# Kernel optimization log

Hardware: AMD Instinct MI355X
Metric: run time of the kernel (lower is better)

## Reference

```python
import jax, jax.numpy as jnp
import numpy as np

COMMITMENT_COST = 0.25

def setup_inputs() -> dict:
    key = jax.random.key(0)
    k1, k2 = jax.random.split(key)
    B, K, D = 32768, 4096, 256
    inputs = jax.random.normal(k1, (B, D), dtype=jnp.float32)
    embedding = jax.random.normal(k2, (K, D), dtype=jnp.float32) * (1.0 / np.sqrt(D))
    return {"inputs": inputs, "embedding": embedding}

def reference(inputs, embedding):
    distances = (
        jnp.sum(inputs * inputs, axis=1, keepdims=True)
        + jnp.sum(embedding * embedding, axis=1)
        - 2.0 * jnp.einsum("bd,kd->bk", inputs, embedding)
    )
    encoding_indices = jnp.argmin(distances, axis=1)  # [B]
    # one-hot @ embedding == gather
    quantized = embedding[encoding_indices]  # [B, D]
    # Eval-mode loss (module in inference mode): q_latent + commitment * e_latent
    e_latent_loss = jnp.mean((inputs - jax.lax.stop_gradient(quantized)) ** 2)
    q_latent_loss = jnp.mean((quantized - jax.lax.stop_gradient(inputs)) ** 2)
    loss = q_latent_loss + COMMITMENT_COST * e_latent_loss
    # Straight-through estimator
    quantized_st = inputs + jax.lax.stop_gradient(quantized - inputs)
    return (quantized_st, loss, encoding_indices)
```

## Files before the change

kernel.cpp:

```cpp
#include <hip/hip_runtime.h>

constexpr int Bsz = 32768;
constexpr int Ksz = 4096;
constexpr int Dsz = 256;

constexpr int KD = 512;
constexpr int NSLABS = 4;
constexpr int CTILES = 8;
constexpr int NCAND = 8;
constexpr int NFBLK = Bsz / 4;
constexpr float TAU = 1e-3f;

typedef __attribute__((ext_vector_type(8))) short short8;
typedef __attribute__((ext_vector_type(4))) float f32x4;

__device__ __forceinline__ unsigned short f2bf(float f) {
  unsigned u = __float_as_uint(f);
  u += 0x7fffu + ((u >> 16) & 1u);
  return (unsigned short)(u >> 16);
}
__device__ __forceinline__ float bf2f(unsigned short h) {
  return __uint_as_float(((unsigned)h) << 16);
}

__global__ __launch_bounds__(256) void vq_prep_x(const float* __restrict__ X,
                                                 unsigned short* __restrict__ X2) {
  const int tid = blockIdx.x * 256 + threadIdx.x;
  const int row = tid >> 6;
  const int d4 = tid & 63;
  const float4 v = *reinterpret_cast<const float4*>(X + (size_t)row * Dsz + d4 * 4);
  ushort4 h, l;
  h.x = f2bf(v.x); l.x = f2bf(v.x - bf2f(h.x));
  h.y = f2bf(v.y); l.y = f2bf(v.y - bf2f(h.y));
  h.z = f2bf(v.z); l.z = f2bf(v.z - bf2f(h.z));
  h.w = f2bf(v.w); l.w = f2bf(v.w - bf2f(h.w));
  *reinterpret_cast<ushort4*>(X2 + (size_t)row * KD + d4 * 4) = h;
  *reinterpret_cast<ushort4*>(X2 + (size_t)row * KD + 256 + d4 * 4) = l;
}

__global__ __launch_bounds__(256) void vq_prep_e(const float* __restrict__ E,
                                                 unsigned short* __restrict__ E2,
                                                 float* __restrict__ enorm) {
  const int wid = threadIdx.x >> 6;
  const int lane = threadIdx.x & 63;
  const int k = blockIdx.x * 4 + wid;
  const float4 v = *reinterpret_cast<const float4*>(E + (size_t)k * Dsz + lane * 4);
  ushort4 h, l;
  h.x = f2bf(v.x); l.x = f2bf(v.x - bf2f(h.x));
  h.y = f2bf(v.y); l.y = f2bf(v.y - bf2f(h.y));
  h.z = f2bf(v.z); l.z = f2bf(v.z - bf2f(h.z));
  h.w = f2bf(v.w); l.w = f2bf(v.w - bf2f(h.w));
  *reinterpret_cast<ushort4*>(E2 + (size_t)k * KD + lane * 4) = h;
  *reinterpret_cast<ushort4*>(E2 + (size_t)k * KD + 256 + lane * 4) = l;
  float s = v.x * v.x + v.y * v.y + v.z * v.z + v.w * v.w;
#pragma unroll
  for (int off = 32; off > 0; off >>= 1) s += __shfl_down(s, off);
  if (lane == 0) enorm[k] = s;
}

__global__ __launch_bounds__(256, 2) void vq_gemm_argmin(
    const unsigned short* __restrict__ X2, const unsigned short* __restrict__ E2,
    const float* __restrict__ enorm, float4* __restrict__ cand) {
  __shared__ unsigned short sA[128 * 64];
  __shared__ unsigned short sB[128 * 64];

  const int t = threadIdx.x;
  const int lane = t & 63;
  const int wid = t >> 6;
  const int wm = wid >> 1, wn = wid & 1;
  const int mb = blockIdx.x & 255;
  const int slab = blockIdx.x >> 8;
  const int row0 = mb * 128;
  const int col0 = slab * 1024;

  const int rr = lane >> 3;
  const int sl = (lane & 7) ^ rr;
  const int sloff = (sl & 3) * 8 + ((sl & 4) << 6);

  const int l15 = lane & 15;
  const int fsel = ((lane >> 4) ^ (lane & 7)) * 8;

  float m1[16], m2[16];
  int i1[16], i2[16];
#pragma unroll
  for (int r = 0; r < 16; ++r) {
    m1[r] = 3.4e38f; m2[r] = 3.4e38f; i1[r] = 0x7fffffff; i2[r] = 0x7fffffff;
  }

  for (int ct = 0; ct < CTILES; ++ct) {
    const int colt = col0 + ct * 128;
    f32x4 acc[4][4];
#pragma unroll
    for (int a = 0; a < 4; ++a)
#pragma unroll
      for (int b = 0; b < 4; ++b) acc[a][b] = f32x4{0.f, 0.f, 0.f, 0.f};

    for (int c = 0; c < 8; ++c) {
      const int kb = c * 32;
      __syncthreads();
      const int rbase = wid * 32;
#pragma unroll
      for (int qi = 0; qi < 4; ++qi) {
        const int r0 = rbase + qi * 8;
        const unsigned short* gA =
            X2 + (size_t)(row0 + r0 + rr) * KD + kb + sloff;
        __builtin_amdgcn_global_load_lds(
            (const __attribute__((address_space(1))) void*)gA,
            (__attribute__((address_space(3))) void*)(sA + r0 * 64), 16, 0, 0);
        const unsigned short* gB =
            E2 + (size_t)(colt + r0 + rr) * KD + kb + sloff;
        __builtin_amdgcn_global_load_lds(
            (const __attribute__((address_space(1))) void*)gB,
            (__attribute__((address_space(3))) void*)(sB + r0 * 64), 16, 0, 0);
      }
      __syncthreads();

      short8 ah[4], bh[4];
#pragma unroll
      for (int a = 0; a < 4; ++a)
        ah[a] = *reinterpret_cast<const short8*>(
            sA + (wm * 64 + a * 16 + l15) * 64 + fsel);
#pragma unroll
      for (int b = 0; b < 4; ++b)
        bh[b] = *reinterpret_cast<const short8*>(
            sB + (wn * 64 + b * 16 + l15) * 64 + fsel);
#pragma unroll
      for (int a = 0; a < 4; ++a)
#pragma unroll
        for (int b = 0; b < 4; ++b)
          acc[a][b] = __builtin_amdgcn_mfma_f32_16x16x32_bf16(ah[a], bh[b], acc[a][b], 0, 0, 0);

      short8 al[4];
#pragma unroll
      for (int a = 0; a < 4; ++a)
        al[a] = *reinterpret_cast<const short8*>(
            sA + (wm * 64 + a * 16 + l15) * 64 + (fsel ^ 32));
#pragma unroll
      for (int a = 0; a < 4; ++a)
#pragma unroll
        for (int b = 0; b < 4; ++b)
          acc[a][b] = __builtin_amdgcn_mfma_f32_16x16x32_bf16(al[a], bh[b], acc[a][b], 0, 0, 0);

      short8 bl[4];
#pragma unroll
      for (int b = 0; b < 4; ++b)
        bl[b] = *reinterpret_cast<const short8*>(
            sB + (wn * 64 + b * 16 + l15) * 64 + (fsel ^ 32));
#pragma unroll
      for (int a = 0; a < 4; ++a)
#pragma unroll
        for (int b = 0; b < 4; ++b)
          acc[a][b] = __builtin_amdgcn_mfma_f32_16x16x32_bf16(ah[a], bl[b], acc[a][b], 0, 0, 0);
    }

#pragma unroll
    for (int b = 0; b < 4; ++b) {
      const int colg = colt + wn * 64 + b * 16 + l15;
      const float en = enorm[colg];
#pragma unroll
      for (int a = 0; a < 4; ++a) {
#pragma unroll
        for (int q = 0; q < 4; ++q) {
          const float s = en - 2.0f * acc[a][b][q];
          const int r = a * 4 + q;
          if (s < m1[r]) {
            m2[r] = m1[r]; i2[r] = i1[r]; m1[r] = s; i1[r] = colg;
          } else if (s < m2[r]) {
            m2[r] = s; i2[r] = colg;
          }
        }
      }
    }
  }

#pragma unroll
  for (int r = 0; r < 16; ++r) {
    float v1 = m1[r], v2 = m2[r];
    int ii1 = i1[r], ii2 = i2[r];
#pragma unroll
    for (int mbit = 1; mbit <= 8; mbit <<= 1) {
      const float ov1 = __shfl_xor(v1, mbit);
      const float ov2 = __shfl_xor(v2, mbit);
      const int oi1 = __shfl_xor(ii1, mbit);
      const int oi2 = __shfl_xor(ii2, mbit);
      if (ov1 < v1 || (ov1 == v1 && oi1 < ii1)) {
        float nv2 = v1; int ni2 = ii1;
        if (ov2 < nv2) { nv2 = ov2; ni2 = oi2; }
        v1 = ov1; ii1 = oi1; v2 = nv2; ii2 = ni2;
      } else if (ov1 < v2) {
        v2 = ov1; ii2 = oi1;
      }
    }
    if (l15 == 0) {
      const int rowg = row0 + wm * 64 + (r >> 2) * 16 + (lane >> 4) * 4 + (r & 3);
      cand[(size_t)rowg * NCAND + slab * 2 + wn] =
          make_float4(v1, __int_as_float(ii1), v2, __int_as_float(ii2));
    }
  }
}

__global__ __launch_bounds__(256) void vq_finalize(
    const float* __restrict__ X, const float* __restrict__ E,
    const float4* __restrict__ cand, float* __restrict__ out,
    float* __restrict__ partial) {
  __shared__ float ls[4];
  const int wid = threadIdx.x >> 6;
  const int lane = threadIdx.x & 63;
  const int b = blockIdx.x * 4 + wid;

  float v1 = 3.4e38f, v2 = 3.4e38f;
  int ii1 = 0x7fffffff, ii2 = 0x7fffffff;
  if (lane < NCAND) {
    const float4 c = cand[(size_t)b * NCAND + lane];
    v1 = c.x; ii1 = __float_as_int(c.y);
    v2 = c.z; ii2 = __float_as_int(c.w);
  }
#pragma unroll
  for (int mbit = 1; mbit <= 4; mbit <<= 1) {
    const float ov1 = __shfl_xor(v1, mbit);
    const float ov2 = __shfl_xor(v2, mbit);
    const int oi1 = __shfl_xor(ii1, mbit);
    const int oi2 = __shfl_xor(ii2, mbit);
    if (ov1 < v1 || (ov1 == v1 && oi1 < ii1)) {
      float nv2 = v1; int ni2 = ii1;
      if (ov2 < nv2) { nv2 = ov2; ni2 = oi2; }
      v1 = ov1; ii1 = oi1; v2 = nv2; ii2 = ni2;
    } else if (ov1 < v2) {
      v2 = ov1; ii2 = oi1;
    }
  }
  v1 = __shfl(v1, 0); v2 = __shfl(v2, 0);
  ii1 = __shfl(ii1, 0); ii2 = __shfl(ii2, 0);

  const float4 x = *reinterpret_cast<const float4*>(X + (size_t)b * Dsz + lane * 4);

  if (v2 - v1 < TAU) {
    const float4 e1 = *reinterpret_cast<const float4*>(E + (size_t)ii1 * Dsz + lane * 4);
    const float4 e2 = *reinterpret_cast<const float4*>(E + (size_t)ii2 * Dsz + lane * 4);
    double d1 = ((double)x.x - e1.x) * ((double)x.x - e1.x) +
                ((double)x.y - e1.y) * ((double)x.y - e1.y) +
                ((double)x.z - e1.z) * ((double)x.z - e1.z) +
                ((double)x.w - e1.w) * ((double)x.w - e1.w);
    double d2 = ((double)x.x - e2.x) * ((double)x.x - e2.x) +
                ((double)x.y - e2.y) * ((double)x.y - e2.y) +
                ((double)x.z - e2.z) * ((double)x.z - e2.z) +
                ((double)x.w - e2.w) * ((double)x.w - e2.w);
#pragma unroll
    for (int mbit = 1; mbit <= 32; mbit <<= 1) {
      d1 += __shfl_xor(d1, mbit);
      d2 += __shfl_xor(d2, mbit);
    }
    if (d2 < d1 || (d2 == d1 && ii2 < ii1)) ii1 = ii2;
  }

  const float4 q = *reinterpret_cast<const float4*>(E + (size_t)ii1 * Dsz + lane * 4);
  *reinterpret_cast<float4*>(out + (size_t)b * Dsz + lane * 4) = q;

  const float dx = x.x - q.x, dy = x.y - q.y, dz = x.z - q.z, dw = x.w - q.w;
  float s2 = dx * dx + dy * dy + dz * dz + dw * dw;
#pragma unroll
  for (int off = 32; off > 0; off >>= 1) s2 += __shfl_down(s2, off);
  if (lane == 0) {
    ls[wid] = s2;
    out[(size_t)Bsz * Dsz + 1 + b] = (float)ii1;
  }
  __syncthreads();
  if (threadIdx.x == 0)
    partial[blockIdx.x] = ls[0] + ls[1] + ls[2] + ls[3];
}

__global__ __launch_bounds__(256) void vq_loss_reduce(const float* __restrict__ partial,
                                                      float* __restrict__ out) {
  __shared__ float ls[4];
  const int wid = threadIdx.x >> 6;
  const int lane = threadIdx.x & 63;
  float s = 0.f;
  for (int i = threadIdx.x; i < NFBLK; i += 256) s += partial[i];
#pragma unroll
  for (int off = 32; off > 0; off >>= 1) s += __shfl_down(s, off);
  if (lane == 0) ls[wid] = s;
  __syncthreads();
  if (threadIdx.x == 0)
    out[(size_t)Bsz * Dsz] = (ls[0] + ls[1] + ls[2] + ls[3]) *
                             (1.25f / ((float)Bsz * (float)Dsz));
}

extern "C" void kernel_launch(void* const* d_in, const int* in_sizes, int n_in,
                              void* d_out, int out_size, void* d_ws, size_t ws_size,
                              hipStream_t stream) {
  const float* X = (const float*)d_in[0];
  const float* E = (const float*)d_in[1];
  float* out = (float*)d_out;

  char* ws = (char*)d_ws;
  float* enorm = (float*)ws;
  unsigned short* X2 = (unsigned short*)(ws + (16 << 10));
  unsigned short* E2 = (unsigned short*)(ws + (16 << 10) + (32 << 20));
  float4* cand = (float4*)(ws + (16 << 10) + (36 << 20));
  float* partial = (float*)(ws + (16 << 10) + (40 << 20));

  vq_prep_x<<<Bsz * 64 / 256, 256, 0, stream>>>(X, X2);
  vq_prep_e<<<Ksz / 4, 256, 0, stream>>>(E, E2, enorm);
  vq_gemm_argmin<<<(Bsz / 128) * NSLABS, 256, 0, stream>>>(X2, E2, enorm, cand);
  vq_finalize<<<NFBLK, 256, 0, stream>>>(X, E, cand, out, partial);
  vq_loss_reduce<<<1, 256, 0, stream>>>(partial, out);
}
```

Before: 384.3 us.

## Restructure argmin GEMM into 256x256 tiles with double-buffered LDS pipeline

The GEMM-argmin kernel moves from 128-row blocks that loop over 1024-column slabs to 512-thread blocks that each compute one 256x256 output tile. LDS staging is double-buffered, with explicit vmcnt waits, barriers and setprio so global-to-LDS loads overlap the MFMAs. The three bf16 split products (hi*hi, lo*hi, hi*lo) are folded into one 12-step K loop through offset macros. Block indices are swizzled for L2 locality, and per-tile top-2 candidates are merged in shared memory, which doubles the candidate count that finalize reduces. The larger tiles raise arithmetic reuse per byte loaded, at the cost of higher register and LDS pressure and a larger candidate buffer.

```diff
diff --git a/kernel.cpp b/kernel.cpp
--- a/kernel.cpp
+++ b/kernel.cpp
@@ -5,9 +5,8 @@
 constexpr int Dsz = 256;
 
 constexpr int KD = 512;
-constexpr int NSLABS = 4;
-constexpr int CTILES = 8;
-constexpr int NCAND = 8;
+constexpr int NT = 12;
+constexpr int NCAND = 16;
 constexpr int NFBLK = Bsz / 4;
 constexpr float TAU = 1e-3f;
 
@@ -58,145 +57,186 @@
   if (lane == 0) enorm[k] = s;
 }
 
-__global__ __launch_bounds__(256, 2) void vq_gemm_argmin(
+__global__ __launch_bounds__(512, 2) void vq_gemm_argmin(
     const unsigned short* __restrict__ X2, const unsigned short* __restrict__ E2,
     const float* __restrict__ enorm, float4* __restrict__ cand) {
-  __shared__ unsigned short sA[128 * 64];
-  __shared__ unsigned short sB[128 * 64];
-
-  const int t = threadIdx.x;
-  const int lane = t & 63;
-  const int wid = t >> 6;
-  const int wm = wid >> 1, wn = wid & 1;
-  const int mb = blockIdx.x & 255;
-  const int slab = blockIdx.x >> 8;
-  const int row0 = mb * 128;
-  const int col0 = slab * 1024;
-
-  const int rr = lane >> 3;
-  const int sl = (lane & 7) ^ rr;
-  const int sloff = (sl & 3) * 8 + ((sl & 4) << 6);
+  __shared__ unsigned short sA[2][256 * 64];
+  __shared__ unsigned short sB[2][256 * 64];
+
+  const int t5 = threadIdx.x;
+  const int lane = t5 & 63;
+  const int wid = t5 >> 6;
+  const int wm = wid >> 2;
+  const int wn = wid & 3;
+
+  const int bid = blockIdx.x;
+  const int swz = (bid & 7) * 256 + (bid >> 3);
+  const int mb = swz >> 4;
+  const int nb = swz & 15;
+  const int row0 = mb * 256;
+  const int col0 = nb * 256;
+
+  const int srow = lane >> 3;
+  const int sslot = (lane & 7) ^ srow;
 
   const int l15 = lane & 15;
-  const int fsel = ((lane >> 4) ^ (lane & 7)) * 8;
-
-  float m1[16], m2[16];
-  int i1[16], i2[16];
-#pragma unroll
-  for (int r = 0; r < 16; ++r) {
-    m1[r] = 3.4e38f; m2[r] = 3.4e38f; i1[r] = 0x7fffffff; i2[r] = 0x7fffffff;
-  }
-
-  for (int ct = 0; ct < CTILES; ++ct) {
-    const int colt = col0 + ct * 128;
-    f32x4 acc[4][4];
-#pragma unroll
-    for (int a = 0; a < 4; ++a)
-#pragma unroll
-      for (int b = 0; b < 4; ++b) acc[a][b] = f32x4{0.f, 0.f, 0.f, 0.f};
-
-    for (int c = 0; c < 8; ++c) {
-      const int kb = c * 32;
-      __syncthreads();
-      const int rbase = wid * 32;
-#pragma unroll
-      for (int qi = 0; qi < 4; ++qi) {
-        const int r0 = rbase + qi * 8;
-        const unsigned short* gA =
-            X2 + (size_t)(row0 + r0 + rr) * KD + kb + sloff;
-        __builtin_amdgcn_global_load_lds(
-            (const __attribute__((address_space(1))) void*)gA,
-            (__attribute__((address_space(3))) void*)(sA + r0 * 64), 16, 0, 0);
-        const unsigned short* gB =
-            E2 + (size_t)(colt + r0 + rr) * KD + kb + sloff;
-        __builtin_amdgcn_global_load_lds(
-            (const __attribute__((address_space(1))) void*)gB,
-            (__attribute__((address_space(3))) void*)(sB + r0 * 64), 16, 0, 0);
+  const int lhi = lane >> 4;
+  const int lx = lane & 7;
+
+  f32x4 acc[8][4];
+#pragma unroll
+  for (int m = 0; m < 8; ++m)
+#pragma unroll
+    for (int n = 0; n < 4; ++n) acc[m][n] = f32x4{0.f, 0.f, 0.f, 0.f};
+
+#define AOF(kt) ((((kt) >> 2) == 1 ? 256 : 0) + ((kt) & 3) * 64)
+#define BOF(kt) ((((kt) >> 2) == 2 ? 256 : 0) + ((kt) & 3) * 64)
+
+#define STAGE(BUFI, AO, BO)                                                    \
+  {                                                                            \
+    _Pragma("unroll") for (int q = 0; q < 4; ++q) {                            \
+      const int r = wid * 32 + q * 8;                                          \
+      __builtin_amdgcn_global_load_lds(                                        \
+          (const __attribute__((address_space(1))) void*)(                     \
+              X2 + (size_t)(row0 + r + srow) * KD + (AO) + sslot * 8),         \
+          (__attribute__((address_space(3))) void*)(&sA[BUFI][r * 64]), 16, 0, 0); \
+    }                                                                          \
+    _Pragma("unroll") for (int q = 0; q < 4; ++q) {                            \
+      const int r = wid * 32 + q * 8;                                          \
+      __builtin_amdgcn_global_load_lds(                                        \
+          (const __attribute__((address_space(1))) void*)(                     \
+              E2 + (size_t)(col0 + r + srow) * KD + (BO) + sslot * 8),         \
+          (__attribute__((address_space(3))) void*)(&sB[BUFI][r * 64]), 16, 0, 0); \
+    }                                                                          \
+  }
+
+#define LOADFRAGS(BUFI, KS)                                                    \
+  {                                                                            \
+    _Pragma("unroll") for (int m = 0; m < 8; ++m)                              \
+        af[m] = *reinterpret_cast<const short8*>(                              \
+            &sA[BUFI][(wm * 128 + m * 16 + l15) * 64 +                         \
+                      (((KS)*4 + lhi) ^ lx) * 8]);                             \
+    _Pragma("unroll") for (int n = 0; n < 4; ++n)                              \
+        bf[n] = *reinterpret_cast<const short8*>(                              \
+            &sB[BUFI][(wn * 64 + n * 16 + l15) * 64 +                          \
+                      (((KS)*4 + lhi) ^ lx) * 8]);                             \
+  }
+
+#define MFMAS                                                                  \
+  {                                                                            \
+    _Pragma("unroll") for (int m = 0; m < 8; ++m)                              \
+        _Pragma("unroll") for (int n = 0; n < 4; ++n)                          \
+            acc[m][n] = __builtin_amdgcn_mfma_f32_16x16x32_bf16(               \
+                af[m], bf[n], acc[m][n], 0, 0, 0);                             \
+  }
+
+  STAGE(0, AOF(0), BOF(0));
+  STAGE(1, AOF(1), BOF(1));
+
+#pragma unroll
+  for (int t = 0; t < NT; ++t) {
+    const int buf = t & 1;
+    short8 af[8], bf[4];
+
+    if (t < NT - 1) {
+      asm volatile("s_waitcnt vmcnt(8)" ::: "memory");
+    } else {
+      asm volatile("s_waitcnt vmcnt(0)" ::: "memory");
+    }
+    __builtin_amdgcn_sched_barrier(0);
+    __builtin_amdgcn_s_barrier();
+    __builtin_amdgcn_sched_barrier(0);
+
+    LOADFRAGS(buf, 0);
+    asm volatile("s_waitcnt lgkmcnt(0)" ::: "memory");
+    __builtin_amdgcn_sched_barrier(0);
+    __builtin_amdgcn_s_setprio(1);
+    MFMAS;
+    __builtin_amdgcn_s_setprio(0);
+
+    LOADFRAGS(buf, 1);
+    asm volatile("s_waitcnt lgkmcnt(0)" ::: "memory");
+    __builtin_amdgcn_sched_barrier(0);
+    __builtin_amdgcn_s_barrier();
+    __builtin_amdgcn_sched_barrier(0);
+
+    if (t + 2 < NT) {
+      STAGE(buf, AOF(t + 2), BOF(t + 2));
+    }
+    __builtin_amdgcn_sched_barrier(0);
+
+    __builtin_amdgcn_s_setprio(1);
+    MFMAS;
+    __builtin_amdgcn_s_setprio(0);
+  }
+
+  __syncthreads();
+
+  float en[4];
+#pragma unroll
+  for (int n = 0; n < 4; ++n) en[n] = enorm[col0 + wn * 64 + n * 16 + l15];
+
+  float4* scr = reinterpret_cast<float4*>(&sA[0][0]);
+
+#pragma unroll
+  for (int m = 0; m < 8; ++m) {
+#pragma unroll
+    for (int q = 0; q < 4; ++q) {
+      float v1 = 3.4e38f, v2 = 3.4e38f;
+      int ii1 = 0x7fffffff, ii2 = 0x7fffffff;
+#pragma unroll
+      for (int n = 0; n < 4; ++n) {
+        const float s = en[n] - 2.0f * acc[m][n][q];
+        const int colg = col0 + wn * 64 + n * 16 + l15;
+        if (s < v1) { v2 = v1; ii2 = ii1; v1 = s; ii1 = colg; }
+        else if (s < v2) { v2 = s; ii2 = colg; }
       }
-      __syncthreads();
-
-      short8 ah[4], bh[4];
-#pragma unroll
-      for (int a = 0; a < 4; ++a)
-        ah[a] = *reinterpret_cast<const short8*>(
-            sA + (wm * 64 + a * 16 + l15) * 64 + fsel);
-#pragma unroll
-      for (int b = 0; b < 4; ++b)
-        bh[b] = *reinterpret_cast<const short8*>(
-            sB + (wn * 64 + b * 16 + l15) * 64 + fsel);
-#pragma unroll
-      for (int a = 0; a < 4; ++a)
-#pragma unroll
-        for (int b = 0; b < 4; ++b)
-          acc[a][b] = __builtin_amdgcn_mfma_f32_16x16x32_bf16(ah[a], bh[b], acc[a][b], 0, 0, 0);
-
-      short8 al[4];
-#pragma unroll
-      for (int a = 0; a < 4; ++a)
-        al[a] = *reinterpret_cast<const short8*>(
-            sA + (wm * 64 + a * 16 + l15) * 64 + (fsel ^ 32));
-#pragma unroll
-      for (int a = 0; a < 4; ++a)
-#pragma unroll
-        for (int b = 0; b < 4; ++b)
-          acc[a][b] = __builtin_amdgcn_mfma_f32_16x16x32_bf16(al[a], bh[b], acc[a][b], 0, 0, 0);
-
-      short8 bl[4];
-#pragma unroll
-      for (int b = 0; b < 4; ++b)
-        bl[b] = *reinterpret_cast<const short8*>(
-            sB + (wn * 64 + b * 16 + l15) * 64 + (fsel ^ 32));
-#pragma unroll
-      for (int a = 0; a < 4; ++a)
-#pragma unroll
-        for (int b = 0; b < 4; ++b)
-          acc[a][b] = __builtin_amdgcn_mfma_f32_16x16x32_bf16(ah[a], bl[b], acc[a][b], 0, 0, 0);
-    }
-
-#pragma unroll
-    for (int b = 0; b < 4; ++b) {
-      const int colg = colt + wn * 64 + b * 16 + l15;
-      const float en = enorm[colg];
-#pragma unroll
-      for (int a = 0; a < 4; ++a) {
-#pragma unroll
-        for (int q = 0; q < 4; ++q) {
-          const float s = en - 2.0f * acc[a][b][q];
-          const int r = a * 4 + q;
-          if (s < m1[r]) {
-            m2[r] = m1[r]; i2[r] = i1[r]; m1[r] = s; i1[r] = colg;
-          } else if (s < m2[r]) {
-            m2[r] = s; i2[r] = colg;
-          }
+#pragma unroll
+      for (int mbit = 1; mbit <= 8; mbit <<= 1) {
+        const float ov1 = __shfl_xor(v1, mbit);
+        const float ov2 = __shfl_xor(v2, mbit);
+        const int oi1 = __shfl_xor(ii1, mbit);
+        const int oi2 = __shfl_xor(ii2, mbit);
+        if (ov1 < v1 || (ov1 == v1 && oi1 < ii1)) {
+          float nv2 = v1; int ni2 = ii1;
+          if (ov2 < nv2) { nv2 = ov2; ni2 = oi2; }
+          v1 = ov1; ii1 = oi1; v2 = nv2; ii2 = ni2;
+        } else if (ov1 < v2) {
+          v2 = ov1; ii2 = oi1;
         }
       }
-    }
-  }
-
-#pragma unroll
-  for (int r = 0; r < 16; ++r) {
-    float v1 = m1[r], v2 = m2[r];
-    int ii1 = i1[r], ii2 = i2[r];
-#pragma unroll
-    for (int mbit = 1; mbit <= 8; mbit <<= 1) {
-      const float ov1 = __shfl_xor(v1, mbit);
-      const float ov2 = __shfl_xor(v2, mbit);
-      const int oi1 = __shfl_xor(ii1, mbit);
-      const int oi2 = __shfl_xor(ii2, mbit);
-      if (ov1 < v1 || (ov1 == v1 && oi1 < ii1)) {
+      if (l15 == 0) {
+        const int rl = wm * 128 + m * 16 + lhi * 4 + q;
+        scr[rl * 4 + wn] = make_float4(v1, __int_as_float(ii1),
+                                       v2, __int_as_float(ii2));
+      }
+    }
+  }
+  __syncthreads();
+  if (t5 < 256) {
+    float v1 = 3.4e38f, v2 = 3.4e38f;
+    int ii1 = 0x7fffffff, ii2 = 0x7fffffff;
+#pragma unroll
+    for (int j = 0; j < 4; ++j) {
+      const float4 c = scr[t5 * 4 + j];
+      const float o1 = c.x, o2 = c.z;
+      const int a1 = __float_as_int(c.y), a2 = __float_as_int(c.w);
+      if (o1 < v1 || (o1 == v1 && a1 < ii1)) {
         float nv2 = v1; int ni2 = ii1;
-        if (ov2 < nv2) { nv2 = ov2; ni2 = oi2; }
-        v1 = ov1; ii1 = oi1; v2 = nv2; ii2 = ni2;
-      } else if (ov1 < v2) {
-        v2 = ov1; ii2 = oi1;
+        if (o2 < nv2) { nv2 = o2; ni2 = a2; }
+        v2 = nv2; ii2 = ni2; v1 = o1; ii1 = a1;
+      } else if (o1 < v2) {
+        v2 = o1; ii2 = a1;
       }
     }
-    if (l15 == 0) {
-      const int rowg = row0 + wm * 64 + (r >> 2) * 16 + (lane >> 4) * 4 + (r & 3);
-      cand[(size_t)rowg * NCAND + slab * 2 + wn] =
-          make_float4(v1, __int_as_float(ii1), v2, __int_as_float(ii2));
-    }
-  }
+    cand[(size_t)(row0 + t5) * NCAND + nb] =
+        make_float4(v1, __int_as_float(ii1), v2, __int_as_float(ii2));
+  }
+#undef AOF
+#undef BOF
+#undef STAGE
+#undef LOADFRAGS
+#undef MFMAS
 }
 
 __global__ __launch_bounds__(256) void vq_finalize(
@@ -216,7 +256,7 @@
     v2 = c.z; ii2 = __float_as_int(c.w);
   }
 #pragma unroll
-  for (int mbit = 1; mbit <= 4; mbit <<= 1) {
+  for (int mbit = 1; mbit <= 8; mbit <<= 1) {
     const float ov1 = __shfl_xor(v1, mbit);
     const float ov2 = __shfl_xor(v2, mbit);
     const int oi1 = __shfl_xor(ii1, mbit);
@@ -297,11 +337,11 @@
   unsigned short* X2 = (unsigned short*)(ws + (16 << 10));
   unsigned short* E2 = (unsigned short*)(ws + (16 << 10) + (32 << 20));
   float4* cand = (float4*)(ws + (16 << 10) + (36 << 20));
-  float* partial = (float*)(ws + (16 << 10) + (40 << 20));
+  float* partial = (float*)(ws + (16 << 10) + (44 << 20));
 
   vq_prep_x<<<Bsz * 64 / 256, 256, 0, stream>>>(X, X2);
   vq_prep_e<<<Ksz / 4, 256, 0, stream>>>(E, E2, enorm);
-  vq_gemm_argmin<<<(Bsz / 128) * NSLABS, 256, 0, stream>>>(X2, E2, enorm, cand);
+  vq_gemm_argmin<<<(Bsz / 256) * (Ksz / 256), 512, 0, stream>>>(X2, E2, enorm, cand);
   vq_finalize<<<NFBLK, 256, 0, stream>>>(X, E, cand, out, partial);
   vq_loss_reduce<<<1, 256, 0, stream>>>(partial, out);
 }
```

Result: slower. 449.4 us (+16.9%).
